# Kernel optimization log

Measured on AMD Instinct MI355X. Metric: run time of the kernel, lower is better.

## Reference

```python
import jax, jax.numpy as jnp
import numpy as np

B, SEQ, D, H, L, DFF, K = 2, 2048, 256, 8, 2, 1024, 3
DK = D // H
EPS = 1e-5
DROP_CONNECT = 0.5  # eval mode: weight * (1 - rate)


def _make_pe():
    pos = np.arange(SEQ)[:, None].astype(np.float32)
    div = np.exp(np.arange(0, D, 2).astype(np.float32) * (-np.log(10000.0) / D))
    pe = np.zeros((SEQ, D), np.float32)
    pe[:, 0::2] = np.sin(pos * div)
    pe[:, 1::2] = np.cos(pos * div)
    return jnp.asarray(pe)


def setup_inputs() -> dict:
    key = jax.random.key(0)
    ks = jax.random.split(key, 16)
    s = 0.02
    d = {
        'x': jax.random.normal(ks[0], (B, SEQ, 1), jnp.float32),
        'conv_w': jax.random.normal(ks[1], (D, 1, K), jnp.float32) * s,
        'conv_b': jnp.zeros((D,), jnp.float32),
        'bn_g': jnp.ones((D,), jnp.float32),
        'bn_b': jnp.zeros((D,), jnp.float32),
        'pe': _make_pe(),
        'qW': jax.random.normal(ks[2], (L, D, D), jnp.float32) * s,
        'qb': jnp.zeros((L, D), jnp.float32),
        'kW': jax.random.normal(ks[3], (L, D, D), jnp.float32) * s,
        'kb': jnp.zeros((L, D), jnp.float32),
        'vW': jax.random.normal(ks[4], (L, D, D), jnp.float32) * s,
        'vb': jnp.zeros((L, D), jnp.float32),
        'oW': jax.random.normal(ks[5], (L, D, D), jnp.float32) * s,
        'ob': jnp.zeros((L, D), jnp.float32),
        'scale': jnp.ones((L,), jnp.float32),
        'td': jnp.ones((L, H), jnp.float32),
        'ln1g': jnp.ones((L, D), jnp.float32),
        'ln1b': jnp.zeros((L, D), jnp.float32),
        'f1W': jax.random.normal(ks[6], (L, DFF, D), jnp.float32) * s,
        'f1b': jnp.zeros((L, DFF), jnp.float32),
        'f2W': jax.random.normal(ks[7], (L, D, DFF), jnp.float32) * s,
        'f2b': jnp.zeros((L, D), jnp.float32),
        'ln2g': jnp.ones((L, D), jnp.float32),
        'ln2b': jnp.zeros((L, D), jnp.float32),
        'outW': jax.random.normal(ks[8], (1, D), jnp.float32) * s,
        'outb': jnp.zeros((1,), jnp.float32),
    }
    return d


def _layernorm(z, g, b):
    m = z.mean(-1, keepdims=True)
    v = ((z - m) ** 2).mean(-1, keepdims=True)
    return (z - m) / jnp.sqrt(v + EPS) * g + b


def reference(x, conv_w, conv_b, bn_g, bn_b, pe, qW, qb, kW, kb, vW, vb, oW, ob,
              scale, td, ln1g, ln1b, f1W, f1b, f2W, f2b, ln2g, ln2b, outW, outb):
    # CNN frontend: [B,S,1] -> [B,1,S] -> conv -> BN(eval) -> relu -> [B,S,D]
    h = jnp.transpose(x, (0, 2, 1))
    h = jax.lax.conv_general_dilated(h, conv_w, (1,), 'SAME',
                                     dimension_numbers=('NCH', 'OIH', 'NCH'))
    h = h + conv_b[None, :, None]
    # BatchNorm eval with running_mean=0, running_var=1
    h = h / jnp.sqrt(1.0 + EPS) * bn_g[None, :, None] + bn_b[None, :, None]
    h = jax.nn.relu(h)
    h = jnp.transpose(h, (0, 2, 1)) + pe[None]

    inv_sqrt_dk = 1.0 / np.sqrt(DK).astype(np.float32)
    key_pos = jnp.arange(SEQ, dtype=h.dtype)  # decay depends on key index only

    for l in range(L):
        q = (h @ qW[l].T + qb[l]).reshape(B, SEQ, H, DK).transpose(0, 2, 1, 3)
        k = (h @ kW[l].T + kb[l]).reshape(B, SEQ, H, DK).transpose(0, 2, 1, 3)
        v = (h @ vW[l].T + vb[l]).reshape(B, SEQ, H, DK).transpose(0, 2, 1, 3)
        scores = jnp.einsum('bhqd,bhkd->bhqk', q, k) * (inv_sqrt_dk * scale[l])
        decay = jnp.exp(-td[l][:, None, None] * key_pos[None, None, :])  # [H,1,S]
        scores = scores * decay[None]
        attn = jax.nn.softmax(scores, axis=-1) * jax.nn.sigmoid(scores)
        ctx = jnp.einsum('bhqk,bhkd->bhqd', attn, v)
        ctx = ctx.transpose(0, 2, 1, 3).reshape(B, SEQ, D)
        h = _layernorm(h + (ctx @ oW[l].T + ob[l]), ln1g[l], ln1b[l])
        ff = jax.nn.relu(h @ f1W[l].T + f1b[l]) @ f2W[l].T + f2b[l]
        h = _layernorm(h + ff, ln2g[l], ln2b[l])

    last = h[:, -1, :]
    # DropConnectLinear in eval: weight * (1 - drop_connect_rate)
    return last @ (outW * (1.0 - DROP_CONNECT)).T + outb
```

## Files before the change

### kernel.cpp

```cpp
#include <hip/hip_runtime.h>
#include <math.h>

#define B_    2
#define SEQ_  2048
#define D_    256
#define H_    8
#define DK_   32
#define L_    2
#define DFF_  1024

#define TD_CUT 44.0f

typedef short  bf16x8 __attribute__((ext_vector_type(8)));
typedef float  f32x4  __attribute__((ext_vector_type(4)));

__device__ __forceinline__ int compute_kcut(float tdv) {
    int kcut = SEQ_;
    if (tdv > 1e-9f) {
        float kc = TD_CUT / tdv;
        kcut = (kc >= (float)SEQ_) ? SEQ_ : ((int)kc + 1);
    }
    int kcr = (kcut + 63) & ~63;
    if (kcr > SEQ_) kcr = SEQ_;
    return kcr;
}

__device__ __forceinline__ unsigned short f2bf(float f) {
    unsigned int u = __float_as_uint(f);
    unsigned int r = u + 0x7FFFu + ((u >> 16) & 1u);
    return (unsigned short)(r >> 16);
}
__device__ __forceinline__ float bf2f(unsigned short u) {
    return __uint_as_float(((unsigned int)u) << 16);
}
__device__ __forceinline__ float bflo(unsigned int u) {
    return __uint_as_float(u << 16);
}
__device__ __forceinline__ float bfhi(unsigned int u) {
    return __uint_as_float(u & 0xFFFF0000u);
}

__device__ __forceinline__ void gload_lds16(const unsigned short* g, unsigned short* l) {
    __builtin_amdgcn_global_load_lds(
        (const __attribute__((address_space(1))) unsigned int*)(const unsigned int*)g,
        (__attribute__((address_space(3))) unsigned int*)(unsigned int*)l,
        16, 0, 0);
}

__global__ __launch_bounds__(256) void prep_kernel(
    const float* __restrict__ x, const float* __restrict__ w,
    const float* __restrict__ cb, const float* __restrict__ bg,
    const float* __restrict__ bb, const float* __restrict__ pe,
    float* __restrict__ h, unsigned short* __restrict__ hbf,
    const float* __restrict__ p0, const float* __restrict__ p1,
    const float* __restrict__ p2, const float* __restrict__ p3,
    const float* __restrict__ p4, const float* __restrict__ p5,
    unsigned short* __restrict__ q0, unsigned short* __restrict__ q1,
    unsigned short* __restrict__ q2, unsigned short* __restrict__ q3,
    unsigned short* __restrict__ q4, unsigned short* __restrict__ q5,
    float* __restrict__ hts0, float* __restrict__ hts1)
{
    int bid = blockIdx.x;
    if (bid < 768) {
        int t = bid * 256 + threadIdx.x;
        const float* src; unsigned short* dst; int base;
        if (t < 65536) {
            int a = t >> 14;
            src = a == 0 ? p0 : a == 1 ? p1 : a == 2 ? p2 : p3;
            dst = a == 0 ? q0 : a == 1 ? q1 : a == 2 ? q2 : q3;
            base = (t & 16383) * 8;
        } else {
            int u = t - 65536;
            int a = u >> 16;
            src = a ? p5 : p4;
            dst = a ? q5 : q4;
            base = (u & 65535) * 8;
        }
        float4 v0 = *(const float4*)(src + base);
        float4 v1 = *(const float4*)(src + base + 4);
        bf16x8 o;
        o[0] = (short)f2bf(v0.x); o[1] = (short)f2bf(v0.y);
        o[2] = (short)f2bf(v0.z); o[3] = (short)f2bf(v0.w);
        o[4] = (short)f2bf(v1.x); o[5] = (short)f2bf(v1.y);
        o[6] = (short)f2bf(v1.z); o[7] = (short)f2bf(v1.w);
        *(bf16x8*)(dst + base) = o;
        return;
    }
    int bid2 = bid - 768;
    int b    = bid2 >> 6;
    int tile = bid2 & 63;
    int d    = threadIdx.x;

    hts1[bid2 * 256 + d] = 0.f;

    const float* xp = x + b * SEQ_;
    float w0 = w[d * 3 + 0], w1v = w[d * 3 + 1], w2v = w[d * 3 + 2];
    float gg  = rsqrtf(1.f + 1e-5f) * bg[d];
    float cbd = cb[d], bbd = bb[d];

    int s0 = tile * 32;
    float xm1 = (s0 > 0) ? xp[s0 - 1] : 0.f;
    float x0v = xp[s0];
    float hsum = 0.f;
#pragma unroll 4
    for (int r = 0; r < 32; ++r) {
        int s = s0 + r;
        float xp1 = (s < SEQ_ - 1) ? xp[s + 1] : 0.f;
        float acc = xm1 * w0 + x0v * w1v + xp1 * w2v + cbd;
        acc = acc * gg + bbd;
        acc = fmaxf(acc, 0.f);
        float v = acc + pe[s * D_ + d];
        size_t idx = ((size_t)(b * SEQ_ + s)) * D_ + d;
        h[idx] = v;
        unsigned short ub = f2bf(v);
        hbf[idx] = ub;
        hsum += bf2f(ub);
        xm1 = x0v; x0v = xp1;
    }
    hts0[(b * 64 + tile) * 256 + d] = hsum;
}

__global__ __launch_bounds__(256) void gemm_qkv(
    const unsigned short* __restrict__ A,
    const unsigned short* __restrict__ W0, const unsigned short* __restrict__ W1,
    const unsigned short* __restrict__ W2,
    const float* __restrict__ b0, const float* __restrict__ b1,
    const float* __restrict__ b2,
    unsigned short* __restrict__ O0, unsigned short* __restrict__ O1,
    unsigned short* __restrict__ O2,
    const float* __restrict__ td_l,
    const float* __restrict__ hts_l, float* __restrict__ vts_g,
    int M, int N, int K)
{
    __shared__ unsigned short As[2][2][2048];
    __shared__ unsigned short Bs[2][2][2048];
    __shared__ float hsc[256];

    int z = blockIdx.z;
    int tid  = threadIdx.x;

    if (z == 3) {
        if (blockIdx.x != 0 || blockIdx.y >= 16) return;
        int hh = blockIdx.y & 7;
        int b  = blockIdx.y >> 3;
        int kcr = compute_kcut(td_l[hh]);
        if (kcr >= SEQ_) return;
        int tcut = kcr >> 5;
        const float* hb = hts_l + (size_t)b * 64 * 256 + tid;
        float s = 0.f;
#pragma unroll
        for (int t = 0; t < 64; ++t) {
            float v = hb[t * 256];
            s += (t >= tcut) ? v : 0.f;
        }
        hsc[tid] = s;
        __syncthreads();
        int j = tid >> 3, e = tid & 7;
        const unsigned short* wrow = W2 + (size_t)(hh * 32 + j) * 256 + e * 32;
        float dot = 0.f;
#pragma unroll
        for (int i = 0; i < 4; ++i) {
            bf16x8 w8 = *(const bf16x8*)(wrow + i * 8);
#pragma unroll
            for (int t2 = 0; t2 < 8; ++t2)
                dot += hsc[e * 32 + i * 8 + t2] * bf2f((unsigned short)w8[t2]);
        }
        dot += __shfl_xor(dot, 1);
        dot += __shfl_xor(dot, 2);
        dot += __shfl_xor(dot, 4);
        if (e == 0)
            vts_g[(b * H_ + hh) * 32 + j] = dot + (float)(SEQ_ - kcr) * b2[hh * 32 + j];
        return;
    }

    int bm = blockIdx.y * 64, bn = blockIdx.x * 64;
    if (z > 0) {
        float tdmin = td_l[0];
#pragma unroll
        for (int i = 1; i < H_; ++i) tdmin = fminf(tdmin, td_l[i]);
        if ((bm & (SEQ_ - 1)) >= compute_kcut(tdmin)) return;
    }
    const unsigned short* W = (z == 0) ? W0 : (z == 1) ? W1 : W2;
    const float* bias = (z == 0) ? b0 : (z == 1) ? b1 : b2;
    unsigned short* C = (z == 0) ? O0 : (z == 1) ? O1 : O2;

    int wave = tid >> 6, lane = tid & 63;
    int wm = (wave & 1) * 32, wn = (wave >> 1) * 32;

    int sr  = tid >> 2;
    int scb = (tid & 3) ^ ((sr >> 1) & 3);
    const unsigned short* aG = A + (size_t)(bm + sr) * K + scb * 8;
    const unsigned short* wG = W + (size_t)(bn + sr) * K + scb * 8;

    int fr = lane & 15;
    int kb = lane >> 4;
    int cbo = (kb ^ ((fr >> 1) & 3)) * 8;
    int oA0 = (wm + fr) * 32 + cbo;
    int oA1 = (wm + 16 + fr) * 32 + cbo;
    int oB0 = (wn + fr) * 32 + cbo;
    int oB1 = (wn + 16 + fr) * 32 + cbo;

    f32x4 acc[2][2];
#pragma unroll
    for (int i = 0; i < 2; ++i)
#pragma unroll
        for (int j = 0; j < 2; ++j) acc[i][j] = (f32x4){0.f, 0.f, 0.f, 0.f};

    auto stage = [&](int s, int dd) {
        gload_lds16(aG + s * 64,      &As[dd][0][tid * 8]);
        gload_lds16(aG + s * 64 + 32, &As[dd][1][tid * 8]);
        gload_lds16(wG + s * 64,      &Bs[dd][0][tid * 8]);
        gload_lds16(wG + s * 64 + 32, &Bs[dd][1][tid * 8]);
    };

    int nst = K >> 6;
    stage(0, 0);
    __syncthreads();
    for (int s = 0; s < nst; ++s) {
        int dd = s & 1;
        if (s + 1 < nst) stage(s + 1, dd ^ 1);
#pragma unroll
        for (int kk = 0; kk < 2; ++kk) {
            bf16x8 a0f = *(const bf16x8*)&As[dd][kk][oA0];
            bf16x8 a1f = *(const bf16x8*)&As[dd][kk][oA1];
            bf16x8 b0f = *(const bf16x8*)&Bs[dd][kk][oB0];
            bf16x8 b1f = *(const bf16x8*)&Bs[dd][kk][oB1];
            acc[0][0] = __builtin_amdgcn_mfma_f32_16x16x32_bf16(a0f, b0f, acc[0][0], 0, 0, 0);
            acc[0][1] = __builtin_amdgcn_mfma_f32_16x16x32_bf16(a0f, b1f, acc[0][1], 0, 0, 0);
            acc[1][0] = __builtin_amdgcn_mfma_f32_16x16x32_bf16(a1f, b0f, acc[1][0], 0, 0, 0);
            acc[1][1] = __builtin_amdgcn_mfma_f32_16x16x32_bf16(a1f, b1f, acc[1][1], 0, 0, 0);
        }
        __syncthreads();
    }

    int crow = (lane >> 4) * 4;
    int ccol = lane & 15;
#pragma unroll
    for (int j = 0; j < 2; ++j) {
        float bj = bias[bn + wn + j * 16 + ccol];
#pragma unroll
        for (int i = 0; i < 2; ++i) {
#pragma unroll
            for (int r = 0; r < 4; ++r) {
                float v = acc[i][j][r] + bj;
                C[(size_t)(bm + wm + i * 16 + crow + r) * N + bn + wn + j * 16 + ccol] = f2bf(v);
            }
        }
    }
}

__global__ __launch_bounds__(256) void attn_kernel(
    const unsigned short* __restrict__ q, const unsigned short* __restrict__ k,
    const unsigned short* __restrict__ v, const float* __restrict__ vts_g,
    unsigned short* __restrict__ ctxbf,
    const float* __restrict__ scale_p, const float* __restrict__ td_l)
{
    int b = blockIdx.z, hh = blockIdx.y;
    int tid = threadIdx.x;
    int wave = tid >> 6, lane = tid & 63;
    int q0r = blockIdx.x * 64;

    float sc  = 0.17677669529663687f * scale_p[0];
    float tdv = td_l[hh];
    int kcr = compute_kcut(tdv);
    int ntiles = kcr >> 6;

    __shared__ unsigned short qt[64 * 32];
    __shared__ unsigned short kt[64 * 32];
    __shared__ unsigned short vtT[32 * 72];
    __shared__ unsigned short pl[64 * 72];
    __shared__ float vts_s[32];

    if (tid < 32) vts_s[tid] = vts_g[(b * H_ + hh) * 32 + tid];

    int srow = tid >> 2, sseg = tid & 3;
    gload_lds16(q + ((size_t)(b * SEQ_ + q0r + srow)) * D_ + hh * DK_ + sseg * 8,
                &qt[tid * 8]);

    int fr = lane & 15, kb = lane >> 4;
    const unsigned short* qfrag = &qt[(wave * 16 + fr) * 32 + kb * 8];

    f32x4 acc_o[2];
    acc_o[0] = (f32x4){0.f, 0.f, 0.f, 0.f};
    acc_o[1] = (f32x4){0.f, 0.f, 0.f, 0.f};
    float lpart[4] = {0.f, 0.f, 0.f, 0.f};

    for (int t = 0; t < ntiles; ++t) {
        int k0 = t * 64;
        if (t > 0) __syncthreads();
        {
            gload_lds16(k + ((size_t)(b * SEQ_ + k0 + srow)) * D_ + hh * DK_ + sseg * 8,
                        &kt[tid * 8]);
            const unsigned short* vp =
                v + ((size_t)(b * SEQ_ + k0 + srow)) * D_ + hh * DK_ + sseg * 8;
            uint4 uv = *(const uint4*)vp;
            unsigned short ve[8];
            ve[0] = (unsigned short)(uv.x); ve[1] = (unsigned short)(uv.x >> 16);
            ve[2] = (unsigned short)(uv.y); ve[3] = (unsigned short)(uv.y >> 16);
            ve[4] = (unsigned short)(uv.z); ve[5] = (unsigned short)(uv.z >> 16);
            ve[6] = (unsigned short)(uv.w); ve[7] = (unsigned short)(uv.w >> 16);
#pragma unroll
            for (int e = 0; e < 8; ++e)
                vtT[(sseg * 8 + e) * 72 + srow] = ve[e];
        }
        __syncthreads();

        f32x4 acc_s[4];
        bf16x8 aq = *(const bf16x8*)qfrag;
#pragma unroll
        for (int kt_i = 0; kt_i < 4; ++kt_i) {
            bf16x8 bk = *(const bf16x8*)&kt[(kt_i * 16 + fr) * 32 + kb * 8];
            acc_s[kt_i] = __builtin_amdgcn_mfma_f32_16x16x32_bf16(
                aq, bk, (f32x4){0.f, 0.f, 0.f, 0.f}, 0, 0, 0);
        }
#pragma unroll
        for (int kt_i = 0; kt_i < 4; ++kt_i) {
#pragma unroll
            for (int r = 0; r < 4; ++r) {
                int key = k0 + kt_i * 16 + fr;
                float sv = acc_s[kt_i][r] * sc * __expf(-tdv * (float)key);
                float e  = __expf(sv);
                float sg = 1.f / (1.f + __expf(-sv));
                lpart[r] += e;
                int qrow = wave * 16 + kb * 4 + r;
                pl[qrow * 72 + kt_i * 16 + fr] = f2bf(e * sg);
            }
        }
        __syncthreads();

#pragma unroll
        for (int ks = 0; ks < 2; ++ks) {
            bf16x8 pa = *(const bf16x8*)&pl[(wave * 16 + fr) * 72 + ks * 32 + kb * 8];
#pragma unroll
            for (int nt = 0; nt < 2; ++nt) {
                bf16x8 vb8 = *(const bf16x8*)&vtT[(nt * 16 + fr) * 72 + ks * 32 + kb * 8];
                acc_o[nt] = __builtin_amdgcn_mfma_f32_16x16x32_bf16(pa, vb8, acc_o[nt], 0, 0, 0);
            }
        }
    }

#pragma unroll
    for (int r = 0; r < 4; ++r) {
        lpart[r] += __shfl_xor(lpart[r], 1);
        lpart[r] += __shfl_xor(lpart[r], 2);
        lpart[r] += __shfl_xor(lpart[r], 4);
        lpart[r] += __shfl_xor(lpart[r], 8);
    }
    float taill = (kcr < SEQ_) ? (float)(SEQ_ - kcr) : 0.f;

#pragma unroll
    for (int nt = 0; nt < 2; ++nt) {
        float vadd = (kcr < SEQ_) ? 0.5f * vts_s[nt * 16 + fr] : 0.f;
#pragma unroll
        for (int r = 0; r < 4; ++r) {
            float invL = 1.f / (lpart[r] + taill);
            float o = (acc_o[nt][r] + vadd) * invL;
            int qrow = q0r + wave * 16 + kb * 4 + r;
            ctxbf[((size_t)(b * SEQ_ + qrow)) * D_ + hh * DK_ + nt * 16 + fr] = f2bf(o);
        }
    }
}

__global__ __launch_bounds__(256) void oproj_ln1(
    const unsigned short* __restrict__ ctx, const unsigned short* __restrict__ wo,
    const float* __restrict__ ob, const float* __restrict__ resid,
    const float* __restrict__ g1, const float* __restrict__ bt1,
    float* __restrict__ h1out, unsigned short* __restrict__ h1bf)
{
    __shared__ unsigned short As[2][512];
    __shared__ unsigned short Bs[2][8192];
    __shared__ float lsum[4][16], lsq[4][16], mean_s[16], inv_s[16];

    int tid = threadIdx.x;
    int wave = tid >> 6, lane = tid & 63;
    int bm = blockIdx.x * 16;
    int fr = lane & 15, kb = lane >> 4;
    int q = kb, cl = fr;
    int swz = (fr >> 1) & 3;

    const unsigned short* gpB[4];
    int dstB[4];
#pragma unroll
    for (int i = 0; i < 4; ++i) {
        int sB = i * 256 + tid;
        int r = sB >> 2, ck = (sB & 3) ^ ((r >> 1) & 3);
        gpB[i] = wo + (size_t)r * 256 + ck * 8;
        dstB[i] = sB * 8;
    }
    const unsigned short* gpA = nullptr;
    if (tid < 64) {
        int r = tid >> 2, ck = (tid & 3) ^ ((r >> 1) & 3);
        gpA = ctx + (size_t)(bm + r) * 256 + ck * 8;
    }

    int oA = fr * 32 + ((kb ^ swz) * 8);
    int oB[4];
#pragma unroll
    for (int t = 0; t < 4; ++t) {
        int n = wave * 64 + t * 16 + fr;
        oB[t] = n * 32 + ((kb ^ swz) * 8);
    }

    f32x4 acc[4];
#pragma unroll
    for (int j = 0; j < 4; ++j) acc[j] = (f32x4){0.f, 0.f, 0.f, 0.f};

    auto stage = [&](int s, int dd) {
#pragma unroll
        for (int i = 0; i < 4; ++i) gload_lds16(gpB[i] + s * 32, &Bs[dd][dstB[i]]);
        if (tid < 64) gload_lds16(gpA + s * 32, &As[dd][tid * 8]);
    };

    stage(0, 0);
    __syncthreads();
    for (int s = 0; s < 8; ++s) {
        int dd = s & 1;
        if (s + 1 < 8) stage(s + 1, dd ^ 1);
        bf16x8 af = *(const bf16x8*)&As[dd][oA];
#pragma unroll
        for (int j = 0; j < 4; ++j)
            acc[j] = __builtin_amdgcn_mfma_f32_16x16x32_bf16(
                af, *(const bf16x8*)&Bs[dd][oB[j]], acc[j], 0, 0, 0);
        __syncthreads();
    }

    float zsum[4] = {0.f, 0.f, 0.f, 0.f}, zsq[4] = {0.f, 0.f, 0.f, 0.f};
    float zv[4][4];
#pragma unroll
    for (int ct = 0; ct < 4; ++ct) {
        int col = wave * 64 + ct * 16 + cl;
        float bj = ob[col];
#pragma unroll
        for (int r = 0; r < 4; ++r) {
            int row = bm + q * 4 + r;
            float z = acc[ct][r] + bj + resid[(size_t)row * 256 + col];
            zv[ct][r] = z;
            zsum[r] += z;
            zsq[r]  += z * z;
        }
    }
#pragma unroll
    for (int r = 0; r < 4; ++r) {
#pragma unroll
        for (int off = 1; off < 16; off <<= 1) {
            zsum[r] += __shfl_xor(zsum[r], off);
            zsq[r]  += __shfl_xor(zsq[r], off);
        }
    }
    if (cl == 0) {
#pragma unroll
        for (int r = 0; r < 4; ++r) {
            lsum[wave][q * 4 + r] = zsum[r];
            lsq[wave][q * 4 + r]  = zsq[r];
        }
    }
    __syncthreads();
    if (tid < 16) {
        float s  = lsum[0][tid] + lsum[1][tid] + lsum[2][tid] + lsum[3][tid];
        float sq = lsq[0][tid] + lsq[1][tid] + lsq[2][tid] + lsq[3][tid];
        float mean = s * (1.f / 256.f);
        float var  = sq * (1.f / 256.f) - mean * mean;
        mean_s[tid] = mean;
        inv_s[tid]  = rsqrtf(var + 1e-5f);
    }
    __syncthreads();

#pragma unroll
    for (int ct = 0; ct < 4; ++ct) {
        int col = wave * 64 + ct * 16 + cl;
        float gc = g1[col], bc = bt1[col];
#pragma unroll
        for (int r = 0; r < 4; ++r) {
            int lr = q * 4 + r;
            float o = (zv[ct][r] - mean_s[lr]) * inv_s[lr] * gc + bc;
            size_t off = (size_t)(bm + lr) * 256 + col;
            h1out[off] = o;
            h1bf[off]  = f2bf(o);
        }
    }
}

__global__ __launch_bounds__(256) void ffn_fused(
    const unsigned short* __restrict__ h1bf, const unsigned short* __restrict__ w1,
    const float* __restrict__ f1b, const unsigned short* __restrict__ w2,
    float* __restrict__ part)
{
    __shared__ unsigned short As[2][1024];
    __shared__ unsigned short Bs[2][8192];
    __shared__ unsigned short ffs[32 * 264];

    int tid = threadIdx.x;
    int wave = tid >> 6, lane = tid & 63;
    int c = blockIdx.x;
    int bm = blockIdx.y * 32;
    int fr = lane & 15, kb = lane >> 4;
    int q = kb, cl = fr;

    const unsigned short* gB1[4];
    const unsigned short* gB2[4];
    int dstB[4];
#pragma unroll
    for (int i = 0; i < 4; ++i) {
        int sB = i * 256 + tid;
        int r = sB >> 2, ck = (sB & 3) ^ ((r >> 1) & 3);
        gB1[i] = w1 + (size_t)(c * 256 + r) * 256 + ck * 8;
        gB2[i] = w2 + (size_t)r * 1024 + c * 256 + ck * 8;
        dstB[i] = sB * 8;
    }
    const unsigned short* gA = nullptr;
    if (tid < 128) {
        int ar = tid >> 2, ack = (tid & 3) ^ ((ar >> 1) & 3);
        gA = h1bf + (size_t)(bm + ar) * 256 + ack * 8;
    }

    int oA1[2], oB[4];
#pragma unroll
    for (int t = 0; t < 2; ++t) {
        int m = t * 16 + fr;
        oA1[t] = m * 32 + ((kb ^ ((m >> 1) & 3)) * 8);
    }
#pragma unroll
    for (int t = 0; t < 4; ++t) {
        int n = wave * 64 + t * 16 + fr;
        oB[t] = n * 32 + ((kb ^ ((n >> 1) & 3)) * 8);
    }

    auto stage1 = [&](int s, int dd) {
#pragma unroll
        for (int i = 0; i < 4; ++i) gload_lds16(gB1[i] + s * 32, &Bs[dd][dstB[i]]);
        if (tid < 128) gload_lds16(gA + s * 32, &As[dd][tid * 8]);
    };
    auto stage2 = [&](int s, int dd) {
#pragma unroll
        for (int i = 0; i < 4; ++i) gload_lds16(gB2[i] + s * 32, &Bs[dd][dstB[i]]);
    };

    f32x4 a1[2][4];
#pragma unroll
    for (int i = 0; i < 2; ++i)
#pragma unroll
        for (int j = 0; j < 4; ++j) a1[i][j] = (f32x4){0.f, 0.f, 0.f, 0.f};

    stage1(0, 0);
    __syncthreads();
    for (int ks = 0; ks < 8; ++ks) {
        int dd = ks & 1;
        if (ks + 1 < 8) stage1(ks + 1, dd ^ 1);
        bf16x8 af[2], bfv[4];
#pragma unroll
        for (int t = 0; t < 2; ++t) af[t] = *(const bf16x8*)&As[dd][oA1[t]];
#pragma unroll
        for (int t = 0; t < 4; ++t) bfv[t] = *(const bf16x8*)&Bs[dd][oB[t]];
#pragma unroll
        for (int i = 0; i < 2; ++i)
#pragma unroll
            for (int j = 0; j < 4; ++j)
                a1[i][j] = __builtin_amdgcn_mfma_f32_16x16x32_bf16(af[i], bfv[j], a1[i][j], 0, 0, 0);
        __syncthreads();
    }

#pragma unroll
    for (int ct = 0; ct < 4; ++ct) {
        int col = wave * 64 + ct * 16 + cl;
        float bj = f1b[c * 256 + col];
#pragma unroll
        for (int rt = 0; rt < 2; ++rt)
#pragma unroll
            for (int r = 0; r < 4; ++r) {
                float v = fmaxf(a1[rt][ct][r] + bj, 0.f);
                ffs[(rt * 16 + q * 4 + r) * 264 + col] = f2bf(v);
            }
    }

    f32x4 a2[2][4];
#pragma unroll
    for (int i = 0; i < 2; ++i)
#pragma unroll
        for (int j = 0; j < 4; ++j) a2[i][j] = (f32x4){0.f, 0.f, 0.f, 0.f};

    stage2(0, 0);
    __syncthreads();
    for (int ks = 0; ks < 8; ++ks) {
        int dd = ks & 1;
        if (ks + 1 < 8) stage2(ks + 1, dd ^ 1);
        bf16x8 af[2], bfv[4];
#pragma unroll
        for (int t = 0; t < 2; ++t)
            af[t] = *(const bf16x8*)&ffs[(t * 16 + fr) * 264 + ks * 32 + kb * 8];
#pragma unroll
        for (int t = 0; t < 4; ++t) bfv[t] = *(const bf16x8*)&Bs[dd][oB[t]];
#pragma unroll
        for (int i = 0; i < 2; ++i)
#pragma unroll
            for (int j = 0; j < 4; ++j)
                a2[i][j] = __builtin_amdgcn_mfma_f32_16x16x32_bf16(af[i], bfv[j], a2[i][j], 0, 0, 0);
        __syncthreads();
    }

#pragma unroll
    for (int ct = 0; ct < 4; ++ct) {
        int col = wave * 64 + ct * 16 + cl;
#pragma unroll
        for (int rt = 0; rt < 2; ++rt)
#pragma unroll
            for (int r = 0; r < 4; ++r)
                part[((size_t)c * 4096 + bm + rt * 16 + q * 4 + r) * 256 + col] = a2[rt][ct][r];
    }
}

__global__ __launch_bounds__(256) void merge_ln2(
    const float* __restrict__ h1, const float* __restrict__ part,
    const float* __restrict__ f2b, const float* __restrict__ g2,
    const float* __restrict__ bt2,
    float* __restrict__ hout, unsigned short* __restrict__ hbf,
    const float* __restrict__ outW, const float* __restrict__ outb,
    float* __restrict__ out, int doFinal,
    float* __restrict__ hts1, int doHts)
{
    __shared__ float red[4][256];

    int wrp = threadIdx.x >> 6;
    int row = blockIdx.x * 4 + wrp;
    int lane = threadIdx.x & 63;
    int d = lane * 4;

    float4 z = *(const float4*)(h1 + (size_t)row * 256 + d);
    float4 b4 = *(const float4*)(f2b + d);
    z.x += b4.x; z.y += b4.y; z.z += b4.z; z.w += b4.w;
#pragma unroll
    for (int c = 0; c < 4; ++c) {
        float4 p = *(const float4*)(part + ((size_t)c * 4096 + row) * 256 + d);
        z.x += p.x; z.y += p.y; z.z += p.z; z.w += p.w;
    }

    float s = z.x + z.y + z.z + z.w;
    float ss = z.x * z.x + z.y * z.y + z.z * z.z + z.w * z.w;
#pragma unroll
    for (int off = 1; off < 64; off <<= 1) {
        s += __shfl_xor(s, off);
        ss += __shfl_xor(ss, off);
    }
    float mean = s * (1.f / 256.f);
    float var = ss * (1.f / 256.f) - mean * mean;
    float inv = rsqrtf(var + 1e-5f);

    float4 g4 = *(const float4*)(g2 + d);
    float4 t4 = *(const float4*)(bt2 + d);
    float4 o;
    o.x = (z.x - mean) * inv * g4.x + t4.x;
    o.y = (z.y - mean) * inv * g4.y + t4.y;
    o.z = (z.z - mean) * inv * g4.z + t4.z;
    o.w = (z.w - mean) * inv * g4.w + t4.w;
    *(float4*)(hout + (size_t)row * 256 + d) = o;
    unsigned short s0 = f2bf(o.x), s1 = f2bf(o.y), s2 = f2bf(o.z), s3 = f2bf(o.w);
    unsigned int u01 = (unsigned)s0 | ((unsigned)s1 << 16);
    unsigned int u23 = (unsigned)s2 | ((unsigned)s3 << 16);
    *(uint2*)&hbf[(size_t)row * 256 + d] = make_uint2(u01, u23);

    if (doHts) {
        *(float4*)&red[wrp][d] = make_float4(bf2f(s0), bf2f(s1), bf2f(s2), bf2f(s3));
        __syncthreads();
        int cidx = threadIdx.x;
        float cs = red[0][cidx] + red[1][cidx] + red[2][cidx] + red[3][cidx];
        int b = blockIdx.x >> 9;
        int tile = (blockIdx.x >> 3) & 63;
        atomicAdd(&hts1[((b << 6) + tile) * 256 + cidx], cs);
    }

    if (doFinal && (row == 2047 || row == 4095)) {
        float4 w4 = *(const float4*)(outW + d);
        float s2f = o.x * w4.x + o.y * w4.y + o.z * w4.z + o.w * w4.w;
#pragma unroll
        for (int off = 1; off < 64; off <<= 1) s2f += __shfl_xor(s2f, off);
        if (lane == 0) out[row >> 11] = s2f * 0.5f + outb[0];
    }
}

extern "C" void kernel_launch(void* const* d_in, const int* in_sizes, int n_in,
                              void* d_out, int out_size, void* d_ws, size_t ws_size,
                              hipStream_t stream)
{
    (void)in_sizes; (void)n_in; (void)out_size; (void)ws_size;
    const float* x      = (const float*)d_in[0];
    const float* conv_w = (const float*)d_in[1];
    const float* conv_b = (const float*)d_in[2];
    const float* bn_g   = (const float*)d_in[3];
    const float* bn_b   = (const float*)d_in[4];
    const float* pe     = (const float*)d_in[5];
    const float* qW     = (const float*)d_in[6];
    const float* qb     = (const float*)d_in[7];
    const float* kW     = (const float*)d_in[8];
    const float* kb     = (const float*)d_in[9];
    const float* vW     = (const float*)d_in[10];
    const float* vb     = (const float*)d_in[11];
    const float* oW     = (const float*)d_in[12];
    const float* ob     = (const float*)d_in[13];
    const float* scale  = (const float*)d_in[14];
    const float* td     = (const float*)d_in[15];
    const float* ln1g   = (const float*)d_in[16];
    const float* ln1b   = (const float*)d_in[17];
    const float* f1W    = (const float*)d_in[18];
    const float* f1b    = (const float*)d_in[19];
    const float* f2W    = (const float*)d_in[20];
    const float* f2b    = (const float*)d_in[21];
    const float* ln2g   = (const float*)d_in[22];
    const float* ln2b   = (const float*)d_in[23];
    const float* outW   = (const float*)d_in[24];
    const float* outb   = (const float*)d_in[25];
    float* out = (float*)d_out;

    float* ws = (float*)d_ws;
    const size_t MT = (size_t)B_ * SEQ_ * D_;
    const size_t HTS = (size_t)B_ * 64 * 256;
    float* h     = ws;
    float* h1    = ws + MT;
    float* part  = ws + 2 * MT;
    float* hts0  = ws + 6 * MT;
    float* hts1  = hts0 + HTS;
    float* vts_g = hts1 + HTS;
    unsigned short* bfb = (unsigned short*)(vts_g + 512);
    unsigned short* h_bf   = bfb;
    unsigned short* ctx_bf = bfb + MT;
    unsigned short* q_bf   = bfb + 2 * MT;
    unsigned short* k_bf   = bfb + 3 * MT;
    unsigned short* v_bf   = bfb + 4 * MT;
    unsigned short* h1_bf  = bfb + 5 * MT;
    unsigned short* wq_bf  = bfb + 6 * MT;
    unsigned short* wk_bf  = wq_bf + MT / 8;
    unsigned short* wv_bf  = wk_bf + MT / 8;
    unsigned short* wo_bf  = wv_bf + MT / 8;
    unsigned short* wf1_bf = wo_bf + MT / 8;
    unsigned short* wf2_bf = wf1_bf + MT / 2;

    const int Mrows = B_ * SEQ_;

    prep_kernel<<<768 + 128, 256, 0, stream>>>(
        x, conv_w, conv_b, bn_g, bn_b, pe, h, h_bf,
        qW, kW, vW, oW, f1W, f2W,
        wq_bf, wk_bf, wv_bf, wo_bf, wf1_bf, wf2_bf, hts0, hts1);

    for (int l = 0; l < L_; ++l) {
        const unsigned short* wq_l  = wq_bf  + (size_t)l * D_ * D_;
        const unsigned short* wk_l  = wk_bf  + (size_t)l * D_ * D_;
        const unsigned short* wv_l  = wv_bf  + (size_t)l * D_ * D_;
        const unsigned short* wo_l  = wo_bf  + (size_t)l * D_ * D_;
        const unsigned short* wf1_l = wf1_bf + (size_t)l * DFF_ * D_;
        const unsigned short* wf2_l = wf2_bf + (size_t)l * DFF_ * D_;
        const float* hts_l = (l == 0) ? hts0 : hts1;

        gemm_qkv<<<dim3(D_ / 64, Mrows / 64, 4), 256, 0, stream>>>(
            h_bf, wq_l, wk_l, wv_l, qb + l * D_, kb + l * D_, vb + l * D_,
            q_bf, k_bf, v_bf, td + l * H_, hts_l, vts_g, Mrows, D_, D_);

        attn_kernel<<<dim3(SEQ_ / 64, H_, B_), 256, 0, stream>>>(
            q_bf, k_bf, v_bf, vts_g, ctx_bf, scale + l, td + l * H_);

        oproj_ln1<<<Mrows / 16, 256, 0, stream>>>(
            ctx_bf, wo_l, ob + l * D_, h,
            ln1g + l * D_, ln1b + l * D_, h1, h1_bf);

        ffn_fused<<<dim3(4, Mrows / 32), 256, 0, stream>>>(
            h1_bf, wf1_l, f1b + l * DFF_, wf2_l, part);

        merge_ln2<<<Mrows / 4, 256, 0, stream>>>(
            h1, part, f2b + l * D_, ln2g + l * D_, ln2b + l * D_,
            h, h_bf, outW, outb, out, (l == L_ - 1) ? 1 : 0,
            hts1, (l == 0) ? 1 : 0);
    }
}
```

Measured before the change: 185.5 us.

## Fuse QKV projection into attention kernel, computing K/V per key tile

Removes the separate QKV GEMM launch and the bf16 q/k/v buffers in global memory. Each attention block now projects its own Q tile once and recomputes the K and V projections for every key tile from h, and also computes the tail-sum vts term locally. This trades memory traffic and one launch for redundant K/V recomputation across the 32 query blocks per head, plus many more syncthreads inside the projection loop.

```diff
diff --git a/kernel.cpp b/kernel.cpp
--- a/kernel.cpp
+++ b/kernel.cpp
@@ -32,12 +32,6 @@
 }
 __device__ __forceinline__ float bf2f(unsigned short u) {
     return __uint_as_float(((unsigned int)u) << 16);
-}
-__device__ __forceinline__ float bflo(unsigned int u) {
-    return __uint_as_float(u << 16);
-}
-__device__ __forceinline__ float bfhi(unsigned int u) {
-    return __uint_as_float(u & 0xFFFF0000u);
 }
 
 __device__ __forceinline__ void gload_lds16(const unsigned short* g, unsigned short* l) {
@@ -120,138 +114,13 @@
     hts0[(b * 64 + tile) * 256 + d] = hsum;
 }
 
-__global__ __launch_bounds__(256) void gemm_qkv(
-    const unsigned short* __restrict__ A,
-    const unsigned short* __restrict__ W0, const unsigned short* __restrict__ W1,
-    const unsigned short* __restrict__ W2,
-    const float* __restrict__ b0, const float* __restrict__ b1,
-    const float* __restrict__ b2,
-    unsigned short* __restrict__ O0, unsigned short* __restrict__ O1,
-    unsigned short* __restrict__ O2,
-    const float* __restrict__ td_l,
-    const float* __restrict__ hts_l, float* __restrict__ vts_g,
-    int M, int N, int K)
-{
-    __shared__ unsigned short As[2][2][2048];
-    __shared__ unsigned short Bs[2][2][2048];
-    __shared__ float hsc[256];
-
-    int z = blockIdx.z;
-    int tid  = threadIdx.x;
-
-    if (z == 3) {
-        if (blockIdx.x != 0 || blockIdx.y >= 16) return;
-        int hh = blockIdx.y & 7;
-        int b  = blockIdx.y >> 3;
-        int kcr = compute_kcut(td_l[hh]);
-        if (kcr >= SEQ_) return;
-        int tcut = kcr >> 5;
-        const float* hb = hts_l + (size_t)b * 64 * 256 + tid;
-        float s = 0.f;
-#pragma unroll
-        for (int t = 0; t < 64; ++t) {
-            float v = hb[t * 256];
-            s += (t >= tcut) ? v : 0.f;
-        }
-        hsc[tid] = s;
-        __syncthreads();
-        int j = tid >> 3, e = tid & 7;
-        const unsigned short* wrow = W2 + (size_t)(hh * 32 + j) * 256 + e * 32;
-        float dot = 0.f;
-#pragma unroll
-        for (int i = 0; i < 4; ++i) {
-            bf16x8 w8 = *(const bf16x8*)(wrow + i * 8);
-#pragma unroll
-            for (int t2 = 0; t2 < 8; ++t2)
-                dot += hsc[e * 32 + i * 8 + t2] * bf2f((unsigned short)w8[t2]);
-        }
-        dot += __shfl_xor(dot, 1);
-        dot += __shfl_xor(dot, 2);
-        dot += __shfl_xor(dot, 4);
-        if (e == 0)
-            vts_g[(b * H_ + hh) * 32 + j] = dot + (float)(SEQ_ - kcr) * b2[hh * 32 + j];
-        return;
-    }
-
-    int bm = blockIdx.y * 64, bn = blockIdx.x * 64;
-    if (z > 0) {
-        float tdmin = td_l[0];
-#pragma unroll
-        for (int i = 1; i < H_; ++i) tdmin = fminf(tdmin, td_l[i]);
-        if ((bm & (SEQ_ - 1)) >= compute_kcut(tdmin)) return;
-    }
-    const unsigned short* W = (z == 0) ? W0 : (z == 1) ? W1 : W2;
-    const float* bias = (z == 0) ? b0 : (z == 1) ? b1 : b2;
-    unsigned short* C = (z == 0) ? O0 : (z == 1) ? O1 : O2;
-
-    int wave = tid >> 6, lane = tid & 63;
-    int wm = (wave & 1) * 32, wn = (wave >> 1) * 32;
-
-    int sr  = tid >> 2;
-    int scb = (tid & 3) ^ ((sr >> 1) & 3);
-    const unsigned short* aG = A + (size_t)(bm + sr) * K + scb * 8;
-    const unsigned short* wG = W + (size_t)(bn + sr) * K + scb * 8;
-
-    int fr = lane & 15;
-    int kb = lane >> 4;
-    int cbo = (kb ^ ((fr >> 1) & 3)) * 8;
-    int oA0 = (wm + fr) * 32 + cbo;
-    int oA1 = (wm + 16 + fr) * 32 + cbo;
-    int oB0 = (wn + fr) * 32 + cbo;
-    int oB1 = (wn + 16 + fr) * 32 + cbo;
-
-    f32x4 acc[2][2];
-#pragma unroll
-    for (int i = 0; i < 2; ++i)
-#pragma unroll
-        for (int j = 0; j < 2; ++j) acc[i][j] = (f32x4){0.f, 0.f, 0.f, 0.f};
-
-    auto stage = [&](int s, int dd) {
-        gload_lds16(aG + s * 64,      &As[dd][0][tid * 8]);
-        gload_lds16(aG + s * 64 + 32, &As[dd][1][tid * 8]);
-        gload_lds16(wG + s * 64,      &Bs[dd][0][tid * 8]);
-        gload_lds16(wG + s * 64 + 32, &Bs[dd][1][tid * 8]);
-    };
-
-    int nst = K >> 6;
-    stage(0, 0);
-    __syncthreads();
-    for (int s = 0; s < nst; ++s) {
-        int dd = s & 1;
-        if (s + 1 < nst) stage(s + 1, dd ^ 1);
-#pragma unroll
-        for (int kk = 0; kk < 2; ++kk) {
-            bf16x8 a0f = *(const bf16x8*)&As[dd][kk][oA0];
-            bf16x8 a1f = *(const bf16x8*)&As[dd][kk][oA1];
-            bf16x8 b0f = *(const bf16x8*)&Bs[dd][kk][oB0];
-            bf16x8 b1f = *(const bf16x8*)&Bs[dd][kk][oB1];
-            acc[0][0] = __builtin_amdgcn_mfma_f32_16x16x32_bf16(a0f, b0f, acc[0][0], 0, 0, 0);
-            acc[0][1] = __builtin_amdgcn_mfma_f32_16x16x32_bf16(a0f, b1f, acc[0][1], 0, 0, 0);
-            acc[1][0] = __builtin_amdgcn_mfma_f32_16x16x32_bf16(a1f, b0f, acc[1][0], 0, 0, 0);
-            acc[1][1] = __builtin_amdgcn_mfma_f32_16x16x32_bf16(a1f, b1f, acc[1][1], 0, 0, 0);
-        }
-        __syncthreads();
-    }
-
-    int crow = (lane >> 4) * 4;
-    int ccol = lane & 15;
-#pragma unroll
-    for (int j = 0; j < 2; ++j) {
-        float bj = bias[bn + wn + j * 16 + ccol];
-#pragma unroll
-        for (int i = 0; i < 2; ++i) {
-#pragma unroll
-            for (int r = 0; r < 4; ++r) {
-                float v = acc[i][j][r] + bj;
-                C[(size_t)(bm + wm + i * 16 + crow + r) * N + bn + wn + j * 16 + ccol] = f2bf(v);
-            }
-        }
-    }
-}
-
-__global__ __launch_bounds__(256) void attn_kernel(
-    const unsigned short* __restrict__ q, const unsigned short* __restrict__ k,
-    const unsigned short* __restrict__ v, const float* __restrict__ vts_g,
+__global__ __launch_bounds__(256) void attn_fused(
+    const unsigned short* __restrict__ hbf,
+    const unsigned short* __restrict__ wq, const unsigned short* __restrict__ wk,
+    const unsigned short* __restrict__ wv,
+    const float* __restrict__ qbp, const float* __restrict__ kbp,
+    const float* __restrict__ vbp,
+    const float* __restrict__ hts_l,
     unsigned short* __restrict__ ctxbf,
     const float* __restrict__ scale_p, const float* __restrict__ td_l)
 {
@@ -259,59 +128,134 @@
     int tid = threadIdx.x;
     int wave = tid >> 6, lane = tid & 63;
     int q0r = blockIdx.x * 64;
+    size_t bq = (size_t)b * SEQ_;
 
     float sc  = 0.17677669529663687f * scale_p[0];
     float tdv = td_l[hh];
     int kcr = compute_kcut(tdv);
     int ntiles = kcr >> 6;
 
-    __shared__ unsigned short qt[64 * 32];
-    __shared__ unsigned short kt[64 * 32];
+    __shared__ unsigned short hq_s[2048];
+    __shared__ unsigned short hk_s[2048];
+    __shared__ unsigned short wq_s[1024];
+    __shared__ unsigned short wk_s[1024];
+    __shared__ unsigned short wv_s[1024];
+    __shared__ unsigned short qt[64 * 40];
+    __shared__ unsigned short kt[64 * 40];
     __shared__ unsigned short vtT[32 * 72];
     __shared__ unsigned short pl[64 * 72];
+    __shared__ float hsc[256];
     __shared__ float vts_s[32];
 
-    if (tid < 32) vts_s[tid] = vts_g[(b * H_ + hh) * 32 + tid];
-
-    int srow = tid >> 2, sseg = tid & 3;
-    gload_lds16(q + ((size_t)(b * SEQ_ + q0r + srow)) * D_ + hh * DK_ + sseg * 8,
-                &qt[tid * 8]);
-
+    if (kcr < SEQ_) {
+        int tcut = kcr >> 5;
+        const float* hb = hts_l + (size_t)b * 64 * 256 + tid;
+        float s = 0.f;
+#pragma unroll
+        for (int t = 0; t < 64; ++t) {
+            float v = hb[t * 256];
+            s += (t >= tcut) ? v : 0.f;
+        }
+        hsc[tid] = s;
+        __syncthreads();
+        int j = tid >> 3, e = tid & 7;
+        const bf16x8* wp = (const bf16x8*)(wv + (size_t)(hh * 32 + j) * 256 + e * 32);
+        float dot = 0.f;
+#pragma unroll
+        for (int i = 0; i < 4; ++i) {
+            bf16x8 w8 = wp[i];
+#pragma unroll
+            for (int t2 = 0; t2 < 8; ++t2)
+                dot += hsc[e * 32 + i * 8 + t2] * bf2f((unsigned short)w8[t2]);
+        }
+        dot += __shfl_xor(dot, 1);
+        dot += __shfl_xor(dot, 2);
+        dot += __shfl_xor(dot, 4);
+        if (e == 0) vts_s[j] = dot + (float)(SEQ_ - kcr) * vbp[hh * 32 + j];
+    }
+
+    int sr = tid >> 2, scb = (tid & 3) ^ ((sr >> 1) & 3);
+    int wtid = tid & 127, wr = wtid >> 2;
+    int wck = (wtid & 3) ^ ((wr >> 1) & 3);
     int fr = lane & 15, kb = lane >> 4;
-    const unsigned short* qfrag = &qt[(wave * 16 + fr) * 32 + kb * 8];
-
-    f32x4 acc_o[2];
-    acc_o[0] = (f32x4){0.f, 0.f, 0.f, 0.f};
-    acc_o[1] = (f32x4){0.f, 0.f, 0.f, 0.f};
+    int cbo = (kb ^ ((fr >> 1) & 3)) * 8;
+    int ccol = fr, crow = kb * 4;
+
+    f32x4 acc_q[2], acc_o[2];
+    acc_q[0] = acc_q[1] = (f32x4){0.f, 0.f, 0.f, 0.f};
+    acc_o[0] = acc_o[1] = (f32x4){0.f, 0.f, 0.f, 0.f};
     float lpart[4] = {0.f, 0.f, 0.f, 0.f};
 
     for (int t = 0; t < ntiles; ++t) {
         int k0 = t * 64;
-        if (t > 0) __syncthreads();
-        {
-            gload_lds16(k + ((size_t)(b * SEQ_ + k0 + srow)) * D_ + hh * DK_ + sseg * 8,
-                        &kt[tid * 8]);
-            const unsigned short* vp =
-                v + ((size_t)(b * SEQ_ + k0 + srow)) * D_ + hh * DK_ + sseg * 8;
-            uint4 uv = *(const uint4*)vp;
-            unsigned short ve[8];
-            ve[0] = (unsigned short)(uv.x); ve[1] = (unsigned short)(uv.x >> 16);
-            ve[2] = (unsigned short)(uv.y); ve[3] = (unsigned short)(uv.y >> 16);
-            ve[4] = (unsigned short)(uv.z); ve[5] = (unsigned short)(uv.z >> 16);
-            ve[6] = (unsigned short)(uv.w); ve[7] = (unsigned short)(uv.w >> 16);
-#pragma unroll
-            for (int e = 0; e < 8; ++e)
-                vtT[(sseg * 8 + e) * 72 + srow] = ve[e];
+        f32x4 acc_k[2], acc_v[2];
+        acc_k[0] = acc_k[1] = (f32x4){0.f, 0.f, 0.f, 0.f};
+        acc_v[0] = acc_v[1] = (f32x4){0.f, 0.f, 0.f, 0.f};
+
+        for (int ks = 0; ks < 8; ++ks) {
+            __syncthreads();
+            if (t == 0)
+                gload_lds16(hbf + (bq + q0r + sr) * 256 + ks * 32 + scb * 8, &hq_s[tid * 8]);
+            gload_lds16(hbf + (bq + k0 + sr) * 256 + ks * 32 + scb * 8, &hk_s[tid * 8]);
+            if (tid < 128) {
+                gload_lds16(wq + (size_t)(hh * 32 + wr) * 256 + ks * 32 + wck * 8, &wq_s[wtid * 8]);
+                gload_lds16(wv + (size_t)(hh * 32 + wr) * 256 + ks * 32 + wck * 8, &wv_s[wtid * 8]);
+            } else {
+                gload_lds16(wk + (size_t)(hh * 32 + wr) * 256 + ks * 32 + wck * 8, &wk_s[wtid * 8]);
+            }
+            __syncthreads();
+
+            bf16x8 ak  = *(const bf16x8*)&hk_s[(wave * 16 + fr) * 32 + cbo];
+            bf16x8 bk0 = *(const bf16x8*)&wk_s[fr * 32 + cbo];
+            bf16x8 bk1 = *(const bf16x8*)&wk_s[(16 + fr) * 32 + cbo];
+            bf16x8 av0 = *(const bf16x8*)&wv_s[fr * 32 + cbo];
+            bf16x8 av1 = *(const bf16x8*)&wv_s[(16 + fr) * 32 + cbo];
+            acc_k[0] = __builtin_amdgcn_mfma_f32_16x16x32_bf16(ak, bk0, acc_k[0], 0, 0, 0);
+            acc_k[1] = __builtin_amdgcn_mfma_f32_16x16x32_bf16(ak, bk1, acc_k[1], 0, 0, 0);
+            acc_v[0] = __builtin_amdgcn_mfma_f32_16x16x32_bf16(av0, ak, acc_v[0], 0, 0, 0);
+            acc_v[1] = __builtin_amdgcn_mfma_f32_16x16x32_bf16(av1, ak, acc_v[1], 0, 0, 0);
+            if (t == 0) {
+                bf16x8 aq  = *(const bf16x8*)&hq_s[(wave * 16 + fr) * 32 + cbo];
+                bf16x8 bq0 = *(const bf16x8*)&wq_s[fr * 32 + cbo];
+                bf16x8 bq1 = *(const bf16x8*)&wq_s[(16 + fr) * 32 + cbo];
+                acc_q[0] = __builtin_amdgcn_mfma_f32_16x16x32_bf16(aq, bq0, acc_q[0], 0, 0, 0);
+                acc_q[1] = __builtin_amdgcn_mfma_f32_16x16x32_bf16(aq, bq1, acc_q[1], 0, 0, 0);
+            }
+        }
+
+        if (t == 0) {
+#pragma unroll
+            for (int n = 0; n < 2; ++n) {
+                float bj = qbp[hh * 32 + n * 16 + ccol];
+#pragma unroll
+                for (int r = 0; r < 4; ++r)
+                    qt[(wave * 16 + crow + r) * 40 + n * 16 + ccol] = f2bf(acc_q[n][r] + bj);
+            }
+        }
+#pragma unroll
+        for (int n = 0; n < 2; ++n) {
+            float bj = kbp[hh * 32 + n * 16 + ccol];
+#pragma unroll
+            for (int r = 0; r < 4; ++r)
+                kt[(wave * 16 + crow + r) * 40 + n * 16 + ccol] = f2bf(acc_k[n][r] + bj);
+        }
+#pragma unroll
+        for (int d = 0; d < 2; ++d) {
+#pragma unroll
+            for (int r = 0; r < 4; ++r) {
+                int dim = d * 16 + crow + r;
+                vtT[dim * 72 + wave * 16 + ccol] = f2bf(acc_v[d][r] + vbp[hh * 32 + dim]);
+            }
         }
         __syncthreads();
 
+        bf16x8 aq8 = *(const bf16x8*)&qt[(wave * 16 + fr) * 40 + kb * 8];
         f32x4 acc_s[4];
-        bf16x8 aq = *(const bf16x8*)qfrag;
 #pragma unroll
         for (int kt_i = 0; kt_i < 4; ++kt_i) {
-            bf16x8 bk = *(const bf16x8*)&kt[(kt_i * 16 + fr) * 32 + kb * 8];
+            bf16x8 bk8 = *(const bf16x8*)&kt[(kt_i * 16 + fr) * 40 + kb * 8];
             acc_s[kt_i] = __builtin_amdgcn_mfma_f32_16x16x32_bf16(
-                aq, bk, (f32x4){0.f, 0.f, 0.f, 0.f}, 0, 0, 0);
+                aq8, bk8, (f32x4){0.f, 0.f, 0.f, 0.f}, 0, 0, 0);
         }
 #pragma unroll
         for (int kt_i = 0; kt_i < 4; ++kt_i) {
@@ -322,18 +266,17 @@
                 float e  = __expf(sv);
                 float sg = 1.f / (1.f + __expf(-sv));
                 lpart[r] += e;
-                int qrow = wave * 16 + kb * 4 + r;
-                pl[qrow * 72 + kt_i * 16 + fr] = f2bf(e * sg);
+                pl[(wave * 16 + crow + r) * 72 + kt_i * 16 + fr] = f2bf(e * sg);
             }
         }
         __syncthreads();
 
 #pragma unroll
-        for (int ks = 0; ks < 2; ++ks) {
-            bf16x8 pa = *(const bf16x8*)&pl[(wave * 16 + fr) * 72 + ks * 32 + kb * 8];
+        for (int ks2 = 0; ks2 < 2; ++ks2) {
+            bf16x8 pa = *(const bf16x8*)&pl[(wave * 16 + fr) * 72 + ks2 * 32 + kb * 8];
 #pragma unroll
             for (int nt = 0; nt < 2; ++nt) {
-                bf16x8 vb8 = *(const bf16x8*)&vtT[(nt * 16 + fr) * 72 + ks * 32 + kb * 8];
+                bf16x8 vb8 = *(const bf16x8*)&vtT[(nt * 16 + fr) * 72 + ks2 * 32 + kb * 8];
                 acc_o[nt] = __builtin_amdgcn_mfma_f32_16x16x32_bf16(pa, vb8, acc_o[nt], 0, 0, 0);
             }
         }
@@ -355,8 +298,8 @@
         for (int r = 0; r < 4; ++r) {
             float invL = 1.f / (lpart[r] + taill);
             float o = (acc_o[nt][r] + vadd) * invL;
-            int qrow = q0r + wave * 16 + kb * 4 + r;
-            ctxbf[((size_t)(b * SEQ_ + qrow)) * D_ + hh * DK_ + nt * 16 + fr] = f2bf(o);
+            int qrow = q0r + wave * 16 + crow + r;
+            ctxbf[(bq + qrow) * D_ + hh * DK_ + nt * 16 + fr] = f2bf(o);
         }
     }
 }
@@ -721,9 +664,6 @@
     unsigned short* bfb = (unsigned short*)(vts_g + 512);
     unsigned short* h_bf   = bfb;
     unsigned short* ctx_bf = bfb + MT;
-    unsigned short* q_bf   = bfb + 2 * MT;
-    unsigned short* k_bf   = bfb + 3 * MT;
-    unsigned short* v_bf   = bfb + 4 * MT;
     unsigned short* h1_bf  = bfb + 5 * MT;
     unsigned short* wq_bf  = bfb + 6 * MT;
     unsigned short* wk_bf  = wq_bf + MT / 8;
@@ -748,12 +688,10 @@
         const unsigned short* wf2_l = wf2_bf + (size_t)l * DFF_ * D_;
         const float* hts_l = (l == 0) ? hts0 : hts1;
 
-        gemm_qkv<<<dim3(D_ / 64, Mrows / 64, 4), 256, 0, stream>>>(
-            h_bf, wq_l, wk_l, wv_l, qb + l * D_, kb + l * D_, vb + l * D_,
-            q_bf, k_bf, v_bf, td + l * H_, hts_l, vts_g, Mrows, D_, D_);
-
-        attn_kernel<<<dim3(SEQ_ / 64, H_, B_), 256, 0, stream>>>(
-            q_bf, k_bf, v_bf, vts_g, ctx_bf, scale + l, td + l * H_);
+        attn_fused<<<dim3(SEQ_ / 64, H_, B_), 256, 0, stream>>>(
+            h_bf, wq_l, wk_l, wv_l,
+            qb + l * D_, kb + l * D_, vb + l * D_,
+            hts_l, ctx_bf, scale + l, td + l * H_);
 
         oproj_ln1<<<Mrows / 16, 256, 0, stream>>>(
             ctx_bf, wo_l, ob + l * D_, h,
```

Measured after the change: 192.8 us. +3.9%, slower.

## Fuse FFN split-K merge and LayerNorm2 into ffn_fused via last-block counter

Applied to the files above, without the earlier changes.

Removes the separate merge_ln2 launch. Each of the four column-chunk blocks for a 32-row tile bumps an atomic counter after writing its partial sums, and the last block to arrive reduces the four partials, adds the residual and bias, applies LayerNorm, and writes h, its bf16 copy, the hts tile sums and the final output. This saves one kernel launch per layer and replaces per-row atomicAdds on hts1 with direct stores. In exchange the merge runs on only 128 blocks at the tail of the FFN, and the scheme depends on the counters being zeroed in prep and on the fence ordering.

```diff
diff --git a/kernel.cpp b/kernel.cpp
--- a/kernel.cpp
+++ b/kernel.cpp
@@ -32,12 +32,6 @@
 }
 __device__ __forceinline__ float bf2f(unsigned short u) {
     return __uint_as_float(((unsigned int)u) << 16);
-}
-__device__ __forceinline__ float bflo(unsigned int u) {
-    return __uint_as_float(u << 16);
-}
-__device__ __forceinline__ float bfhi(unsigned int u) {
-    return __uint_as_float(u & 0xFFFF0000u);
 }
 
 __device__ __forceinline__ void gload_lds16(const unsigned short* g, unsigned short* l) {
@@ -58,10 +52,12 @@
     unsigned short* __restrict__ q0, unsigned short* __restrict__ q1,
     unsigned short* __restrict__ q2, unsigned short* __restrict__ q3,
     unsigned short* __restrict__ q4, unsigned short* __restrict__ q5,
-    float* __restrict__ hts0, float* __restrict__ hts1)
+    float* __restrict__ hts0, float* __restrict__ hts1,
+    unsigned int* __restrict__ cnt)
 {
     int bid = blockIdx.x;
     if (bid < 768) {
+        if (bid == 0 && threadIdx.x < 128) cnt[threadIdx.x] = 0u;
         int t = bid * 256 + threadIdx.x;
         const float* src; unsigned short* dst; int base;
         if (t < 65536) {
@@ -483,11 +479,19 @@
 __global__ __launch_bounds__(256) void ffn_fused(
     const unsigned short* __restrict__ h1bf, const unsigned short* __restrict__ w1,
     const float* __restrict__ f1b, const unsigned short* __restrict__ w2,
-    float* __restrict__ part)
+    float* __restrict__ part,
+    const float* __restrict__ h1, const float* __restrict__ f2b,
+    const float* __restrict__ g2, const float* __restrict__ bt2,
+    float* __restrict__ hout, unsigned short* __restrict__ hbf,
+    const float* __restrict__ outW, const float* __restrict__ outb,
+    float* __restrict__ out, int doFinal,
+    float* __restrict__ hts1, int doHts,
+    unsigned int* __restrict__ cnt, int target)
 {
     __shared__ unsigned short As[2][1024];
     __shared__ unsigned short Bs[2][8192];
     __shared__ unsigned short ffs[32 * 264];
+    __shared__ unsigned oldv_s;
 
     int tid = threadIdx.x;
     int wave = tid >> 6, lane = tid & 63;
@@ -606,73 +610,70 @@
             for (int r = 0; r < 4; ++r)
                 part[((size_t)c * 4096 + bm + rt * 16 + q * 4 + r) * 256 + col] = a2[rt][ct][r];
     }
-}
-
-__global__ __launch_bounds__(256) void merge_ln2(
-    const float* __restrict__ h1, const float* __restrict__ part,
-    const float* __restrict__ f2b, const float* __restrict__ g2,
-    const float* __restrict__ bt2,
-    float* __restrict__ hout, unsigned short* __restrict__ hbf,
-    const float* __restrict__ outW, const float* __restrict__ outb,
-    float* __restrict__ out, int doFinal,
-    float* __restrict__ hts1, int doHts)
-{
-    __shared__ float red[4][256];
-
-    int wrp = threadIdx.x >> 6;
-    int row = blockIdx.x * 4 + wrp;
-    int lane = threadIdx.x & 63;
-    int d = lane * 4;
-
-    float4 z = *(const float4*)(h1 + (size_t)row * 256 + d);
-    float4 b4 = *(const float4*)(f2b + d);
-    z.x += b4.x; z.y += b4.y; z.z += b4.z; z.w += b4.w;
-#pragma unroll
-    for (int c = 0; c < 4; ++c) {
-        float4 p = *(const float4*)(part + ((size_t)c * 4096 + row) * 256 + d);
-        z.x += p.x; z.y += p.y; z.z += p.z; z.w += p.w;
-    }
-
-    float s = z.x + z.y + z.z + z.w;
-    float ss = z.x * z.x + z.y * z.y + z.z * z.z + z.w * z.w;
-#pragma unroll
-    for (int off = 1; off < 64; off <<= 1) {
-        s += __shfl_xor(s, off);
-        ss += __shfl_xor(ss, off);
-    }
-    float mean = s * (1.f / 256.f);
-    float var = ss * (1.f / 256.f) - mean * mean;
-    float inv = rsqrtf(var + 1e-5f);
-
-    float4 g4 = *(const float4*)(g2 + d);
-    float4 t4 = *(const float4*)(bt2 + d);
-    float4 o;
-    o.x = (z.x - mean) * inv * g4.x + t4.x;
-    o.y = (z.y - mean) * inv * g4.y + t4.y;
-    o.z = (z.z - mean) * inv * g4.z + t4.z;
-    o.w = (z.w - mean) * inv * g4.w + t4.w;
-    *(float4*)(hout + (size_t)row * 256 + d) = o;
-    unsigned short s0 = f2bf(o.x), s1 = f2bf(o.y), s2 = f2bf(o.z), s3 = f2bf(o.w);
-    unsigned int u01 = (unsigned)s0 | ((unsigned)s1 << 16);
-    unsigned int u23 = (unsigned)s2 | ((unsigned)s3 << 16);
-    *(uint2*)&hbf[(size_t)row * 256 + d] = make_uint2(u01, u23);
+
+    __threadfence();
+    __syncthreads();
+    if (tid == 0) oldv_s = atomicAdd(&cnt[blockIdx.y], 1u);
+    __syncthreads();
+    if (oldv_s != (unsigned)target) return;
+    __threadfence();
+
+    float* hsumL = (float*)ffs;
+    float4 csum = make_float4(0.f, 0.f, 0.f, 0.f);
+    int dcol = lane * 4;
+    for (int rr = 0; rr < 8; ++rr) {
+        int row = bm + wave * 8 + rr;
+        float4 z = *(const float4*)(h1 + (size_t)row * 256 + dcol);
+        float4 b4 = *(const float4*)(f2b + dcol);
+        z.x += b4.x; z.y += b4.y; z.z += b4.z; z.w += b4.w;
+#pragma unroll
+        for (int cc = 0; cc < 4; ++cc) {
+            float4 p = *(const float4*)(part + ((size_t)cc * 4096 + row) * 256 + dcol);
+            z.x += p.x; z.y += p.y; z.z += p.z; z.w += p.w;
+        }
+        float s = z.x + z.y + z.z + z.w;
+        float ss = z.x * z.x + z.y * z.y + z.z * z.z + z.w * z.w;
+#pragma unroll
+        for (int off = 1; off < 64; off <<= 1) {
+            s += __shfl_xor(s, off);
+            ss += __shfl_xor(ss, off);
+        }
+        float mean = s * (1.f / 256.f);
+        float var  = ss * (1.f / 256.f) - mean * mean;
+        float inv  = rsqrtf(var + 1e-5f);
+
+        float4 g4 = *(const float4*)(g2 + dcol);
+        float4 t4 = *(const float4*)(bt2 + dcol);
+        float4 o;
+        o.x = (z.x - mean) * inv * g4.x + t4.x;
+        o.y = (z.y - mean) * inv * g4.y + t4.y;
+        o.z = (z.z - mean) * inv * g4.z + t4.z;
+        o.w = (z.w - mean) * inv * g4.w + t4.w;
+        *(float4*)(hout + (size_t)row * 256 + dcol) = o;
+        unsigned short s0 = f2bf(o.x), s1 = f2bf(o.y), s2 = f2bf(o.z), s3 = f2bf(o.w);
+        *(uint2*)&hbf[(size_t)row * 256 + dcol] =
+            make_uint2((unsigned)s0 | ((unsigned)s1 << 16),
+                       (unsigned)s2 | ((unsigned)s3 << 16));
+        csum.x += bf2f(s0); csum.y += bf2f(s1);
+        csum.z += bf2f(s2); csum.w += bf2f(s3);
+
+        if (doFinal && (row == 2047 || row == 4095)) {
+            float4 w4 = *(const float4*)(outW + dcol);
+            float s2f = o.x * w4.x + o.y * w4.y + o.z * w4.z + o.w * w4.w;
+#pragma unroll
+            for (int off = 1; off < 64; off <<= 1) s2f += __shfl_xor(s2f, off);
+            if (lane == 0) out[row >> 11] = s2f * 0.5f + outb[0];
+        }
+    }
 
     if (doHts) {
-        *(float4*)&red[wrp][d] = make_float4(bf2f(s0), bf2f(s1), bf2f(s2), bf2f(s3));
-        __syncthreads();
-        int cidx = threadIdx.x;
-        float cs = red[0][cidx] + red[1][cidx] + red[2][cidx] + red[3][cidx];
-        int b = blockIdx.x >> 9;
-        int tile = (blockIdx.x >> 3) & 63;
-        atomicAdd(&hts1[((b << 6) + tile) * 256 + cidx], cs);
-    }
-
-    if (doFinal && (row == 2047 || row == 4095)) {
-        float4 w4 = *(const float4*)(outW + d);
-        float s2f = o.x * w4.x + o.y * w4.y + o.z * w4.z + o.w * w4.w;
-#pragma unroll
-        for (int off = 1; off < 64; off <<= 1) s2f += __shfl_xor(s2f, off);
-        if (lane == 0) out[row >> 11] = s2f * 0.5f + outb[0];
+        __syncthreads();
+        *(float4*)&hsumL[wave * 256 + dcol] = csum;
+        __syncthreads();
+        float cs = hsumL[0 * 256 + tid] + hsumL[1 * 256 + tid]
+                 + hsumL[2 * 256 + tid] + hsumL[3 * 256 + tid];
+        int bb = blockIdx.y >> 6, tile = blockIdx.y & 63;
+        hts1[((bb << 6) + tile) * 256 + tid] = cs;
     }
 }
 
@@ -718,7 +719,8 @@
     float* hts0  = ws + 6 * MT;
     float* hts1  = hts0 + HTS;
     float* vts_g = hts1 + HTS;
-    unsigned short* bfb = (unsigned short*)(vts_g + 512);
+    unsigned int* cnt = (unsigned int*)(vts_g + 512);
+    unsigned short* bfb = (unsigned short*)(cnt + 128);
     unsigned short* h_bf   = bfb;
     unsigned short* ctx_bf = bfb + MT;
     unsigned short* q_bf   = bfb + 2 * MT;
@@ -737,7 +739,7 @@
     prep_kernel<<<768 + 128, 256, 0, stream>>>(
         x, conv_w, conv_b, bn_g, bn_b, pe, h, h_bf,
         qW, kW, vW, oW, f1W, f2W,
-        wq_bf, wk_bf, wv_bf, wo_bf, wf1_bf, wf2_bf, hts0, hts1);
+        wq_bf, wk_bf, wv_bf, wo_bf, wf1_bf, wf2_bf, hts0, hts1, cnt);
 
     for (int l = 0; l < L_; ++l) {
         const unsigned short* wq_l  = wq_bf  + (size_t)l * D_ * D_;
@@ -760,11 +762,10 @@
             ln1g + l * D_, ln1b + l * D_, h1, h1_bf);
 
         ffn_fused<<<dim3(4, Mrows / 32), 256, 0, stream>>>(
-            h1_bf, wf1_l, f1b + l * DFF_, wf2_l, part);
-
-        merge_ln2<<<Mrows / 4, 256, 0, stream>>>(
-            h1, part, f2b + l * D_, ln2g + l * D_, ln2b + l * D_,
+            h1_bf, wf1_l, f1b + l * DFF_, wf2_l, part,
+            h1, f2b + l * D_, ln2g + l * D_, ln2b + l * D_,
             h, h_bf, outW, outb, out, (l == L_ - 1) ? 1 : 0,
-            hts1, (l == 0) ? 1 : 0);
-    }
-}
+            hts1, (l == 0) ? 1 : 0,
+            cnt, l * 4 + 3);
+    }
+}
```

New measurement: 368.1 us. 1.98x slower.
